# Kernel tuning notes

Measured on AMD Instinct MI355X. Metric: run time of the kernel, lower is better.

Reference implementation:

```python
import jax, jax.numpy as jnp
import numpy as np

B, C, H = 16, 512, 32
HID, NB, S, P, SR = 512, 36, 26, 7, 2
SCALE = 32.0
N_LOC, N_LOC_LAB = 12, 8
N_GRP, GRP_SZ, N_GRP_LAB = 4, 6, 16
IN_DIM = P * P * C


def roi_align(feat, coords, scale, pooled, sr):
    # feat: (B,C,H,W); coords: (B,NB,4) normalized xyxy. torchvision roi_align,
    # aligned=False, fixed sampling_ratio=sr (adaptive ratio is data-dependent).
    Bs, Cc, Hh, Ww = feat.shape
    x1 = coords[..., 0] * scale
    y1 = coords[..., 1] * scale
    x2 = coords[..., 2] * scale
    y2 = coords[..., 3] * scale
    rw = jnp.maximum(x2 - x1, 1.0)
    rh = jnp.maximum(y2 - y1, 1.0)
    bw = rw / pooled
    bh = rh / pooled
    # sample offsets within roi, in bin units: (pooled*sr,)
    off = (jnp.arange(pooled)[:, None] + (jnp.arange(sr) + 0.5) / sr).reshape(-1)
    ys = y1[..., None] + off * bh[..., None]  # (B,NB,pooled*sr)
    xs = x1[..., None] + off * bw[..., None]

    def prep(t, size):
        valid = (t > -1.0) & (t < size)
        tc = jnp.clip(t, 0.0, size - 1)
        lo = jnp.floor(tc).astype(jnp.int32)
        hi = jnp.minimum(lo + 1, size - 1)
        frac = tc - lo
        return lo, hi, frac, valid

    y_lo, y_hi, ly, vy = prep(ys, Hh)
    x_lo, x_hi, lx, vx = prep(xs, Ww)
    hy, hx = 1.0 - ly, 1.0 - lx

    featl = feat.transpose(0, 2, 3, 1)  # (B,H,W,C)
    b_idx = jnp.arange(Bs)[:, None, None, None]

    def gather(yi, xi):
        # -> (B,NB,Py,Px,C)
        return featl[b_idx, yi[:, :, :, None], xi[:, :, None, :]]

    def w(a, b):
        return (a[..., :, None] * b[..., None, :])[..., None]

    val = (gather(y_lo, x_lo) * w(hy, hx) + gather(y_lo, x_hi) * w(hy, lx)
           + gather(y_hi, x_lo) * w(ly, hx) + gather(y_hi, x_hi) * w(ly, lx))
    mask = (vy[:, :, :, None] & vx[:, :, None, :])[..., None]
    val = jnp.where(mask, val, 0.0)
    val = val.reshape(Bs, -1, pooled, sr, pooled, sr, Cc).mean(axis=(3, 5))
    return val.transpose(0, 1, 4, 2, 3)  # (B,NB,C,pooled,pooled)


def setup_inputs() -> dict:
    key = jax.random.key(0)
    ks = jax.random.split(key, 10)
    lf = jax.random.normal(ks[0], (B, C, H, H), dtype=jnp.float32)
    xs = jnp.sort(jax.random.uniform(ks[1], (B, S, 2)), axis=-1)
    ys = jnp.sort(jax.random.uniform(ks[2], (B, S, 2)), axis=-1)
    coords = jnp.stack([xs[..., 0], ys[..., 0], xs[..., 1], ys[..., 1]], axis=-1)
    sc = 0.02
    return {
        'local_features': lf,
        'pred_bbox_coords': coords,
        'roi_fc_W': jax.random.normal(ks[3], (HID, IN_DIM), dtype=jnp.float32) * sc,
        'roi_fc_b': jnp.zeros((HID,), jnp.float32),
        'coords_W': jax.random.normal(ks[4], (S, 4, HID), dtype=jnp.float32) * sc,
        'coords_b': jnp.zeros((S, 4), jnp.float32),
        'pres_W': jax.random.normal(ks[5], (S, HID), dtype=jnp.float32) * sc,
        'pres_b': jnp.zeros((S,), jnp.float32),
        'loc_W': jax.random.normal(ks[6], (N_LOC, N_LOC_LAB, HID), dtype=jnp.float32) * sc,
        'loc_b': jnp.zeros((N_LOC, N_LOC_LAB), jnp.float32),
        'grp_W': jax.random.normal(ks[7], (N_GRP, N_GRP_LAB, GRP_SZ * HID), dtype=jnp.float32) * sc,
        'grp_b': jnp.zeros((N_GRP, N_GRP_LAB), jnp.float32),
        'loc_idx': jnp.arange(N_LOC, dtype=jnp.int32),
        'grp_idx': jnp.arange(N_GRP * GRP_SZ, dtype=jnp.int32).reshape(N_GRP, GRP_SZ),
    }


def reference(local_features, pred_bbox_coords, roi_fc_W, roi_fc_b, coords_W,
              coords_b, pres_W, pres_b, loc_W, loc_b, grp_W, grp_b, loc_idx, grp_idx):
    Bs = local_features.shape[0]
    # boxes S..NB default to the full image (0,0,1,1)
    full = jnp.broadcast_to(jnp.array([0.0, 0.0, 1.0, 1.0], jnp.float32), (Bs, NB, 4))
    coords_all = full.at[:, :S].set(pred_bbox_coords)
    roi = roi_align(local_features, coords_all, SCALE, P, SR)  # (B,NB,C,P,P)
    flat = roi.reshape(Bs, NB, IN_DIM)
    feats = jax.nn.relu(jnp.einsum('bnf,hf->bnh', flat, roi_fc_W) + roi_fc_b)
    sup = feats[:, :S]  # (B,S,HID)
    # per-box coord refinement heads
    deltas = jnp.einsum('bsh,soh->bso', sup, coords_W) + coords_b  # (B,S,4)
    w = pred_bbox_coords[..., 2] - pred_bbox_coords[..., 0]
    h = pred_bbox_coords[..., 3] - pred_bbox_coords[..., 1]
    wh = jnp.stack([w, h, w, h], axis=-1)
    refined = pred_bbox_coords + deltas * wh
    presence = jnp.einsum('bsh,sh->bs', sup, pres_W) + pres_b  # (B,S)
    # per-box MLC heads
    loc = jnp.einsum('blh,loh->blo', feats[:, loc_idx], loc_W) + loc_b
    # per-group MLC heads (concat box feats within group along hidden)
    gf = feats[:, grp_idx].reshape(Bs, N_GRP, GRP_SZ * HID)
    grp = jnp.einsum('bgk,gok->bgo', gf, grp_W) + grp_b
    mlc = jnp.concatenate([loc.reshape(Bs, -1), grp.reshape(Bs, -1)], axis=1)
    return refined, presence, mlc
```

## Files before the change

kernel.cpp:

```cpp
#include <hip/hip_runtime.h>

typedef unsigned short u16;
typedef __attribute__((ext_vector_type(8))) short short8;
typedef __attribute__((ext_vector_type(8))) unsigned short ushort8_t;
typedef __attribute__((ext_vector_type(4))) float f32x4;
typedef __attribute__((ext_vector_type(2))) float v2f;

#define BATCH   16
#define CCH     512
#define NBOX    36
#define SS      26
#define INDIM   25088
#define HIDN    512
#define M_ROWS  416
#define KSPLIT  56
#define KITERS  7
#define NKB     392

__device__ __forceinline__ u16 f2bf(float f) {
  unsigned u = __float_as_uint(f);
  u += 0x7FFF + ((u >> 16) & 1);
  return (u16)(u >> 16);
}
__device__ __forceinline__ float bf2f(u16 h) {
  return __uint_as_float(((unsigned)h) << 16);
}
__device__ __forceinline__ v2f bf2x2(u16 a, u16 b) {
  v2f r;
  r.x = __uint_as_float(((unsigned)a) << 16);
  r.y = __uint_as_float(((unsigned)b) << 16);
  return r;
}

__global__ __launch_bounds__(256) void k_prep(const float* __restrict__ lf,
                                              const float* __restrict__ roiW,
                                              u16* __restrict__ lf_t,
                                              u16* __restrict__ Wb2) {
  __shared__ union {
    u16 tr[32][66];
    u16 cv[49 * 132];
  } sm;
  int j = blockIdx.x;
  int t = threadIdx.x;

  if (j < 4096) {
    int ct = j & 7, y = (j >> 3) & 31, b = j >> 8;
    int cl = t >> 2;
    int xq = (t & 3) * 8;
    const float* src = lf + ((size_t)(b * CCH + ct * 64 + cl) * 1024) + y * 32 + xq;
    float4 v0 = *(const float4*)src;
    float4 v1 = *(const float4*)(src + 4);
    sm.tr[xq + 0][cl] = f2bf(v0.x); sm.tr[xq + 1][cl] = f2bf(v0.y);
    sm.tr[xq + 2][cl] = f2bf(v0.z); sm.tr[xq + 3][cl] = f2bf(v0.w);
    sm.tr[xq + 4][cl] = f2bf(v1.x); sm.tr[xq + 5][cl] = f2bf(v1.y);
    sm.tr[xq + 6][cl] = f2bf(v1.z); sm.tr[xq + 7][cl] = f2bf(v1.w);
    __syncthreads();
    int xl = t >> 3;
    int cq = (t & 7) * 8;
    ushort8_t o;
#pragma unroll
    for (int i = 0; i < 8; ++i) o[i] = sm.tr[xl][cq + i];
    *(ushort8_t*)(lf_t + ((size_t)b * 1024 + y * 32 + xl) * CCH + ct * 64 + cq) = o;
  } else {
    int j2 = j - 4096;
    int h  = j2 >> 2;
    int c0 = (j2 & 3) * 128;
    const float4* s4 = (const float4*)(roiW + (size_t)h * INDIM + (size_t)c0 * 49);
    for (int i = t; i < 1568; i += 256) {
      float4 v = s4[i];
      int k = i * 4;
#pragma unroll
      for (int jj = 0; jj < 4; ++jj) {
        int kk = k + jj;
        int cc = kk / 49;
        int p  = kk - cc * 49;
        sm.cv[p * 132 + cc] = f2bf((&v.x)[jj]);
      }
    }
    __syncthreads();
    for (int q = t; q < 784; q += 256) {
      int p = q >> 4;
      int cc0 = (q & 15) * 8;
      const u16* sp = &sm.cv[p * 132 + cc0];
      ushort8_t o;
#pragma unroll
      for (int i = 0; i < 8; ++i) o[i] = sp[i];
      int c   = c0 + cc0;
      int kb  = p * 8 + (c >> 6);
      int col = c & 63;
      *(ushort8_t*)(Wb2 + ((size_t)kb * HIDN + h) * 64 + col) = o;
    }
  }
}

__global__ __launch_bounds__(512) void k_roi(const u16* __restrict__ lf_t,
                                             const float* __restrict__ pred,
                                             u16* __restrict__ flat2) {
  __shared__ int   s_ylo[14], s_yhi[14], s_xlo[14], s_xhi[14];
  __shared__ float s_wyl[14], s_wyh[14], s_wxl[14], s_wxh[14];

  int bid = blockIdx.x;
  int xcd = bid & 7;
  int s = bid >> 3;
  int b = xcd * 2 + (s >= 26 ? 1 : 0);
  int n = (s >= 26) ? s - 26 : s;
  int blk = b * 26 + n;
  int t = threadIdx.x;

  if (t < 28) {
    bool isY = t < 14;
    int j = isY ? t : t - 14;
    const float* p = pred + ((size_t)(b * SS + n)) * 4;
    float c0 = p[0], c1 = p[1], c2 = p[2], c3 = p[3];
    float lo1 = (isY ? c1 : c0) * 32.f;
    float hi1 = (isY ? c3 : c2) * 32.f;
    float sz = fmaxf(hi1 - lo1, 1.f);
    float bs = sz * (1.f / 7.f);
    float off = (float)(j >> 1) + 0.25f + 0.5f * (float)(j & 1);
    float pos = lo1 + off * bs;
    bool valid = (pos > -1.f) && (pos < 32.f);
    float tc = fminf(fmaxf(pos, 0.f), 31.f);
    int lo = (int)floorf(tc);
    int hi = min(lo + 1, 31);
    float fr = tc - (float)lo;
    float wl = valid ? (1.f - fr) : 0.f;
    float wh = valid ? fr : 0.f;
    if (isY) { s_ylo[j] = lo; s_yhi[j] = hi; s_wyl[j] = wl; s_wyh[j] = wh; }
    else     { s_xlo[j] = lo; s_xhi[j] = hi; s_wxl[j] = wl; s_wxh[j] = wh; }
  }
  __syncthreads();

  int cg = t & 63;
  int pg = t >> 6;
  const u16* base = lf_t + (size_t)b * 1024 * CCH + cg * 8;

  for (int p = pg; p < 49; p += 8) {
    int py = p / 7, px = p % 7;
    v2f a0 = {0.f, 0.f}, a1 = {0.f, 0.f}, a2 = {0.f, 0.f}, a3 = {0.f, 0.f};
#pragma unroll
    for (int sy = 0; sy < 2; ++sy) {
      int jy = 2 * py + sy;
      const u16* rlo = base + s_ylo[jy] * 32 * CCH;
      const u16* rhi = base + s_yhi[jy] * 32 * CCH;
      float wyl = s_wyl[jy], wyh = s_wyh[jy];
#pragma unroll
      for (int sx = 0; sx < 2; ++sx) {
        int jx = 2 * px + sx;
        int xl = s_xlo[jx] * CCH, xh = s_xhi[jx] * CCH;
        v2f wll = {wyl * s_wxl[jx], wyl * s_wxl[jx]};
        v2f wlh = {wyl * s_wxh[jx], wyl * s_wxh[jx]};
        v2f whl = {wyh * s_wxl[jx], wyh * s_wxl[jx]};
        v2f whh = {wyh * s_wxh[jx], wyh * s_wxh[jx]};
        ushort8_t vll = *(const ushort8_t*)(rlo + xl);
        ushort8_t vlh = *(const ushort8_t*)(rlo + xh);
        ushort8_t vhl = *(const ushort8_t*)(rhi + xl);
        ushort8_t vhh = *(const ushort8_t*)(rhi + xh);
        a0 += wll * bf2x2(vll[0], vll[1]) + wlh * bf2x2(vlh[0], vlh[1])
            + whl * bf2x2(vhl[0], vhl[1]) + whh * bf2x2(vhh[0], vhh[1]);
        a1 += wll * bf2x2(vll[2], vll[3]) + wlh * bf2x2(vlh[2], vlh[3])
            + whl * bf2x2(vhl[2], vhl[3]) + whh * bf2x2(vhh[2], vhh[3]);
        a2 += wll * bf2x2(vll[4], vll[5]) + wlh * bf2x2(vlh[4], vlh[5])
            + whl * bf2x2(vhl[4], vhl[5]) + whh * bf2x2(vhh[4], vhh[5]);
        a3 += wll * bf2x2(vll[6], vll[7]) + wlh * bf2x2(vlh[6], vlh[7])
            + whl * bf2x2(vhl[6], vhl[7]) + whh * bf2x2(vhh[6], vhh[7]);
      }
    }
    ushort8_t o;
    o[0] = f2bf(a0.x * 0.25f); o[1] = f2bf(a0.y * 0.25f);
    o[2] = f2bf(a1.x * 0.25f); o[3] = f2bf(a1.y * 0.25f);
    o[4] = f2bf(a2.x * 0.25f); o[5] = f2bf(a2.y * 0.25f);
    o[6] = f2bf(a3.x * 0.25f); o[7] = f2bf(a3.y * 0.25f);
    int kb = p * 8 + (cg >> 3);
    int col = (cg & 7) * 8;
    *(ushort8_t*)(flat2 + ((size_t)kb * M_ROWS + blk) * 64 + col) = o;
  }
}

__global__ __launch_bounds__(256) void k_gemm(const u16* __restrict__ flat2,
                                              const u16* __restrict__ Wb2,
                                              u16* __restrict__ partials) {
  __shared__ u16 As[128 * 64];
  __shared__ u16 Bs[128 * 64];

  int tid = threadIdx.x;
  int wave = tid >> 6, lane = tid & 63;
  int wm = wave >> 1, wn = wave & 1;
  int quad = lane >> 4, r = lane & 15;
  int xb = r & 7;

  int bid = blockIdx.x;
  int xcd = bid & 7;
  int slot = bid >> 3;
  int z = xcd * 7 + (slot >> 4);
  int xy = slot & 15;
  int tileN0 = (xy & 3) * 128;
  int tileM0 = (xy >> 2) * 128;
  int kb0 = z * KITERS;

  size_t aoff[4], boff[4];
  int    ldso[4];
#pragma unroll
  for (int t = 0; t < 4; ++t) {
    int chunk = (wave * 4 + t) * 64 + lane;
    int row = chunk >> 3;
    int lc = chunk & 7;
    ldso[t] = row * 64 + ((lc ^ (row & 7)) << 3);
    int grow = min(tileM0 + row, M_ROWS - 1);
    aoff[t] = ((size_t)kb0 * M_ROWS + grow) * 64 + lc * 8;
    boff[t] = ((size_t)kb0 * HIDN + tileN0 + row) * 64 + lc * 8;
  }

  f32x4 acc[4][4];
#pragma unroll
  for (int mi = 0; mi < 4; ++mi)
#pragma unroll
    for (int ni = 0; ni < 4; ++ni) acc[mi][ni] = (f32x4){0.f, 0.f, 0.f, 0.f};

  short8 ra[4], rb[4];
#pragma unroll
  for (int t = 0; t < 4; ++t) {
    ra[t] = *(const short8*)(flat2 + aoff[t]);
    rb[t] = *(const short8*)(Wb2 + boff[t]);
  }

  for (int kt = 0; kt < KITERS; ++kt) {
#pragma unroll
    for (int t = 0; t < 4; ++t) {
      *(short8*)&As[ldso[t]] = ra[t];
      *(short8*)&Bs[ldso[t]] = rb[t];
    }
    __syncthreads();

    if (kt + 1 < KITERS) {
      size_t ak = (size_t)(kt + 1) * (M_ROWS * 64);
      size_t bk = (size_t)(kt + 1) * (HIDN * 64);
#pragma unroll
      for (int t = 0; t < 4; ++t) {
        ra[t] = *(const short8*)(flat2 + aoff[t] + ak);
        rb[t] = *(const short8*)(Wb2 + boff[t] + bk);
      }
    }

#pragma unroll
    for (int kk = 0; kk < 64; kk += 32) {
      int k8 = kk >> 3;
      int pc = ((k8 + quad) ^ xb) << 3;
      short8 af[4], bfr[4];
#pragma unroll
      for (int mi = 0; mi < 4; ++mi)
        af[mi] = *(const short8*)&As[(wm * 64 + mi * 16 + r) * 64 + pc];
#pragma unroll
      for (int ni = 0; ni < 4; ++ni)
        bfr[ni] = *(const short8*)&Bs[(wn * 64 + ni * 16 + r) * 64 + pc];
#pragma unroll
      for (int mi = 0; mi < 4; ++mi)
#pragma unroll
        for (int ni = 0; ni < 4; ++ni)
          acc[mi][ni] = __builtin_amdgcn_mfma_f32_16x16x32_bf16(
              af[mi], bfr[ni], acc[mi][ni], 0, 0, 0);
    }
    __syncthreads();
  }

  u16* part = partials + (size_t)z * (M_ROWS * HIDN);
#pragma unroll
  for (int mi = 0; mi < 4; ++mi)
#pragma unroll
    for (int ni = 0; ni < 4; ++ni) {
      int row0 = tileM0 + wm * 64 + mi * 16 + quad * 4;
      int col = tileN0 + wn * 64 + ni * 16 + r;
#pragma unroll
      for (int reg = 0; reg < 4; ++reg) {
        int row = row0 + reg;
        if (row < M_ROWS) part[(size_t)row * HIDN + col] = f2bf(acc[mi][ni][reg]);
      }
    }
}

__global__ __launch_bounds__(256) void k_reduce(const u16* __restrict__ partials,
                                                const float* __restrict__ bias,
                                                float* __restrict__ feats) {
  int gid = blockIdx.x * 256 + threadIdx.x;
  int zh  = gid & 1;
  int idx = gid >> 1;
  int row = idx >> 6;
  int c0  = (idx & 63) * 8;
  float s[8] = {0.f, 0.f, 0.f, 0.f, 0.f, 0.f, 0.f, 0.f};
  const u16* p = partials + (size_t)row * HIDN + c0
               + (size_t)(zh * 28) * (M_ROWS * HIDN);
  for (int z = 0; z < 28; ++z) {
    ushort8_t v = *(const ushort8_t*)(p + (size_t)z * (M_ROWS * HIDN));
#pragma unroll
    for (int j = 0; j < 8; ++j) s[j] += bf2f(v[j]);
  }
#pragma unroll
  for (int j = 0; j < 8; ++j) s[j] += __shfl_xor(s[j], 1);
  if (zh == 0) {
    float4 o0, o1;
    const float* bi = bias + c0;
    o0.x = fmaxf(s[0] + bi[0], 0.f); o0.y = fmaxf(s[1] + bi[1], 0.f);
    o0.z = fmaxf(s[2] + bi[2], 0.f); o0.w = fmaxf(s[3] + bi[3], 0.f);
    o1.x = fmaxf(s[4] + bi[4], 0.f); o1.y = fmaxf(s[5] + bi[5], 0.f);
    o1.z = fmaxf(s[6] + bi[6], 0.f); o1.w = fmaxf(s[7] + bi[7], 0.f);
    float* dst = feats + (size_t)row * HIDN + c0;
    *(float4*)dst = o0;
    *(float4*)(dst + 4) = o1;
  }
}

__device__ __forceinline__ float wave_red(float s) {
#pragma unroll
  for (int off = 32; off > 0; off >>= 1) s += __shfl_down(s, off);
  return s;
}

__device__ __forceinline__ float dot512(const float* __restrict__ f,
                                        const float* __restrict__ w, int lane) {
  const float4* f4 = (const float4*)f;
  const float4* w4 = (const float4*)w;
  float4 x0 = f4[lane], y0 = w4[lane];
  float4 x1 = f4[lane + 64], y1 = w4[lane + 64];
  return x0.x * y0.x + x0.y * y0.y + x0.z * y0.z + x0.w * y0.w +
         x1.x * y1.x + x1.y * y1.y + x1.z * y1.z + x1.w * y1.w;
}

__global__ __launch_bounds__(256) void k_heads(const float* __restrict__ feats,
                                               const float* __restrict__ pred,
                                               const float* __restrict__ cW,
                                               const float* __restrict__ cb,
                                               const float* __restrict__ pW,
                                               const float* __restrict__ pb,
                                               const float* __restrict__ lW,
                                               const float* __restrict__ lb,
                                               const float* __restrict__ gW,
                                               const float* __restrict__ gb,
                                               const int* __restrict__ lidx,
                                               const int* __restrict__ gidx,
                                               float* __restrict__ out) {
  int wid = blockIdx.x * 4 + (threadIdx.x >> 6);
  int lane = threadIdx.x & 63;
  float sum = 0.f;

  if (wid < 1664) {
    int b = wid / 104, rr = wid % 104, s = rr >> 2, o = rr & 3;
    sum = dot512(feats + (size_t)(b * 26 + s) * HIDN,
                 cW + (size_t)(s * 4 + o) * HIDN, lane);
    sum = wave_red(sum);
    if (lane == 0) {
      const float* p = pred + (size_t)(b * SS + s) * 4;
      float wdt = p[2] - p[0], hgt = p[3] - p[1];
      float whv = (o & 1) ? hgt : wdt;
      out[wid] = p[o] + (sum + cb[s * 4 + o]) * whv;
    }
  } else if (wid < 2080) {
    int i = wid - 1664;
    int b = i / 26, s = i % 26;
    sum = dot512(feats + (size_t)(b * 26 + s) * HIDN,
                 pW + (size_t)s * HIDN, lane);
    sum = wave_red(sum);
    if (lane == 0) out[1664 + i] = sum + pb[s];
  } else if (wid < 3616) {
    int i = wid - 2080;
    int b = i / 96, rr = i % 96, l = rr >> 3, o = rr & 7;
    sum = dot512(feats + (size_t)(b * 26 + lidx[l]) * HIDN,
                 lW + (size_t)(l * 8 + o) * HIDN, lane);
    sum = wave_red(sum);
    if (lane == 0) out[2080 + b * 160 + rr] = sum + lb[l * 8 + o];
  } else {
    int i = wid - 3616;
    int b = i / 64, rr = i % 64, g = rr >> 4, o = rr & 15;
    const float* w = gW + (size_t)(g * 16 + o) * 3072;
#pragma unroll
    for (int jj = 0; jj < 6; ++jj) {
      sum += dot512(feats + (size_t)(b * 26 + gidx[g * 6 + jj]) * HIDN,
                    w + jj * 512, lane);
    }
    sum = wave_red(sum);
    if (lane == 0) out[2080 + b * 160 + 96 + rr] = sum + gb[g * 16 + o];
  }
}

extern "C" void kernel_launch(void* const* d_in, const int* in_sizes, int n_in,
                              void* d_out, int out_size, void* d_ws, size_t ws_size,
                              hipStream_t stream) {
  const float* lf      = (const float*)d_in[0];
  const float* pred    = (const float*)d_in[1];
  const float* roiW    = (const float*)d_in[2];
  const float* roiB    = (const float*)d_in[3];
  const float* cW      = (const float*)d_in[4];
  const float* cb      = (const float*)d_in[5];
  const float* pW      = (const float*)d_in[6];
  const float* pb      = (const float*)d_in[7];
  const float* lW      = (const float*)d_in[8];
  const float* lb      = (const float*)d_in[9];
  const float* gW      = (const float*)d_in[10];
  const float* gb      = (const float*)d_in[11];
  const int*   lidx    = (const int*)d_in[12];
  const int*   gidx    = (const int*)d_in[13];
  float* out = (float*)d_out;

  char* ws = (char*)d_ws;
  u16*   lf_t     = (u16*)ws;
  u16*   partials = (u16*)ws;
  u16*   Wb2   = (u16*)(ws + 33030144);
  u16*   flat2 = (u16*)(ws + 33030144 + 25690112);
  float* feats = (float*)(ws + 33030144 + 25690112 + 28901376);

  k_prep<<<6144, 256, 0, stream>>>(lf, roiW, lf_t, Wb2);
  k_roi<<<M_ROWS, 512, 0, stream>>>(lf_t, pred, flat2);
  k_gemm<<<896, 256, 0, stream>>>(flat2, Wb2, partials);
  k_reduce<<<208, 256, 0, stream>>>(partials, roiB, feats);
  k_heads<<<1160, 256, 0, stream>>>(feats, pred, cW, cb, pW, pb, lW, lb, gW, gb,
                                    lidx, gidx, out);
}
```

Baseline: 192.4 us.

## Fuse ROI-align into prep kernel with per-batch semaphores for overlap

Merges the ROI-align kernel into the transpose/convert prep kernel. ROI blocks spin on a per-batch atomic counter until all 256 transpose blocks for that batch have finished, and each box is split into two half-blocks. The W conversion blocks are placed after the ROI blocks so they can overlap the wait. This removes a kernel launch boundary and lets ROI work start per batch, at the cost of a memset launch and spin-wait blocks that depend on the scheduler dispatching blocks in order.

```diff
diff --git a/kernel.cpp b/kernel.cpp
--- a/kernel.cpp
+++ b/kernel.cpp
@@ -32,13 +32,20 @@
   return r;
 }
 
-__global__ __launch_bounds__(256) void k_prep(const float* __restrict__ lf,
-                                              const float* __restrict__ roiW,
-                                              u16* __restrict__ lf_t,
-                                              u16* __restrict__ Wb2) {
+__global__ __launch_bounds__(256) void k_prep_roi(const float* __restrict__ lf,
+                                                  const float* __restrict__ roiW,
+                                                  const float* __restrict__ pred,
+                                                  u16* __restrict__ lf_t,
+                                                  u16* __restrict__ Wb2,
+                                                  u16* __restrict__ flat2,
+                                                  unsigned* __restrict__ sem) {
   __shared__ union {
     u16 tr[32][66];
     u16 cv[49 * 132];
+    struct {
+      int   ylo[14], yhi[14], xlo[14], xhi[14];
+      float wyl[14], wyh[14], wxl[14], wxh[14];
+    } roi;
   } sm;
   int j = blockIdx.x;
   int t = threadIdx.x;
@@ -61,8 +68,102 @@
 #pragma unroll
     for (int i = 0; i < 8; ++i) o[i] = sm.tr[xl][cq + i];
     *(ushort8_t*)(lf_t + ((size_t)b * 1024 + y * 32 + xl) * CCH + ct * 64 + cq) = o;
+    __syncthreads();
+    if (t == 0) {
+      __threadfence();
+      __hip_atomic_fetch_add(sem + b * 32, 1u,
+                             __ATOMIC_RELAXED, __HIP_MEMORY_SCOPE_AGENT);
+    }
+  } else if (j < 4928) {
+    int jj = j - 4096;
+    int half = (jj >= 416) ? 1 : 0;
+    int bj   = half ? jj - 416 : jj;
+    int xcd  = bj & 7;
+    int s    = bj >> 3;
+    int b    = xcd * 2 + (s >= 26 ? 1 : 0);
+    int n    = (s >= 26) ? s - 26 : s;
+    int blk  = b * 26 + n;
+
+    if (t == 0) {
+      while (__hip_atomic_load(sem + b * 32, __ATOMIC_RELAXED,
+                               __HIP_MEMORY_SCOPE_AGENT) < 256u)
+        __builtin_amdgcn_s_sleep(16);
+      __threadfence();
+    }
+    __syncthreads();
+
+    if (t < 28) {
+      bool isY = t < 14;
+      int jt = isY ? t : t - 14;
+      const float* pp = pred + ((size_t)(b * SS + n)) * 4;
+      float c0 = pp[0], c1 = pp[1], c2 = pp[2], c3 = pp[3];
+      float lo1 = (isY ? c1 : c0) * 32.f;
+      float hi1 = (isY ? c3 : c2) * 32.f;
+      float sz = fmaxf(hi1 - lo1, 1.f);
+      float bs = sz * (1.f / 7.f);
+      float off = (float)(jt >> 1) + 0.25f + 0.5f * (float)(jt & 1);
+      float pos = lo1 + off * bs;
+      bool valid = (pos > -1.f) && (pos < 32.f);
+      float tc = fminf(fmaxf(pos, 0.f), 31.f);
+      int lo = (int)floorf(tc);
+      int hi = min(lo + 1, 31);
+      float fr = tc - (float)lo;
+      float wl = valid ? (1.f - fr) : 0.f;
+      float wh = valid ? fr : 0.f;
+      if (isY) { sm.roi.ylo[jt] = lo; sm.roi.yhi[jt] = hi;
+                 sm.roi.wyl[jt] = wl; sm.roi.wyh[jt] = wh; }
+      else     { sm.roi.xlo[jt] = lo; sm.roi.xhi[jt] = hi;
+                 sm.roi.wxl[jt] = wl; sm.roi.wxh[jt] = wh; }
+    }
+    __syncthreads();
+
+    int cgi = t & 63;
+    int pg  = t >> 6;
+    const u16* base = lf_t + (size_t)b * 1024 * CCH + cgi * 8;
+    int pend = half ? 49 : 24;
+
+    for (int p = (half ? 24 : 0) + pg; p < pend; p += 4) {
+      int py = p / 7, px = p % 7;
+      v2f a0 = {0.f, 0.f}, a1 = {0.f, 0.f}, a2 = {0.f, 0.f}, a3 = {0.f, 0.f};
+#pragma unroll
+      for (int sy = 0; sy < 2; ++sy) {
+        int jy = 2 * py + sy;
+        const u16* rlo = base + sm.roi.ylo[jy] * 32 * CCH;
+        const u16* rhi = base + sm.roi.yhi[jy] * 32 * CCH;
+        float wyl = sm.roi.wyl[jy], wyh = sm.roi.wyh[jy];
+#pragma unroll
+        for (int sx = 0; sx < 2; ++sx) {
+          int jx = 2 * px + sx;
+          int xl = sm.roi.xlo[jx] * CCH, xh = sm.roi.xhi[jx] * CCH;
+          v2f wll = {wyl * sm.roi.wxl[jx], wyl * sm.roi.wxl[jx]};
+          v2f wlh = {wyl * sm.roi.wxh[jx], wyl * sm.roi.wxh[jx]};
+          v2f whl = {wyh * sm.roi.wxl[jx], wyh * sm.roi.wxl[jx]};
+          v2f whh = {wyh * sm.roi.wxh[jx], wyh * sm.roi.wxh[jx]};
+          ushort8_t vll = *(const ushort8_t*)(rlo + xl);
+          ushort8_t vlh = *(const ushort8_t*)(rlo + xh);
+          ushort8_t vhl = *(const ushort8_t*)(rhi + xl);
+          ushort8_t vhh = *(const ushort8_t*)(rhi + xh);
+          a0 += wll * bf2x2(vll[0], vll[1]) + wlh * bf2x2(vlh[0], vlh[1])
+              + whl * bf2x2(vhl[0], vhl[1]) + whh * bf2x2(vhh[0], vhh[1]);
+          a1 += wll * bf2x2(vll[2], vll[3]) + wlh * bf2x2(vlh[2], vlh[3])
+              + whl * bf2x2(vhl[2], vhl[3]) + whh * bf2x2(vhh[2], vhh[3]);
+          a2 += wll * bf2x2(vll[4], vll[5]) + wlh * bf2x2(vlh[4], vlh[5])
+              + whl * bf2x2(vhl[4], vhl[5]) + whh * bf2x2(vhh[4], vhh[5]);
+          a3 += wll * bf2x2(vll[6], vll[7]) + wlh * bf2x2(vlh[6], vlh[7])
+              + whl * bf2x2(vhl[6], vhl[7]) + whh * bf2x2(vhh[6], vhh[7]);
+        }
+      }
+      ushort8_t o;
+      o[0] = f2bf(a0.x * 0.25f); o[1] = f2bf(a0.y * 0.25f);
+      o[2] = f2bf(a1.x * 0.25f); o[3] = f2bf(a1.y * 0.25f);
+      o[4] = f2bf(a2.x * 0.25f); o[5] = f2bf(a2.y * 0.25f);
+      o[6] = f2bf(a3.x * 0.25f); o[7] = f2bf(a3.y * 0.25f);
+      int kb  = p * 8 + (cgi >> 3);
+      int col = (cgi & 7) * 8;
+      *(ushort8_t*)(flat2 + ((size_t)kb * M_ROWS + blk) * 64 + col) = o;
+    }
   } else {
-    int j2 = j - 4096;
+    int j2 = j - 4928;
     int h  = j2 >> 2;
     int c0 = (j2 & 3) * 128;
     const float4* s4 = (const float4*)(roiW + (size_t)h * INDIM + (size_t)c0 * 49);
@@ -90,89 +191,6 @@
       int col = c & 63;
       *(ushort8_t*)(Wb2 + ((size_t)kb * HIDN + h) * 64 + col) = o;
     }
-  }
-}
-
-__global__ __launch_bounds__(512) void k_roi(const u16* __restrict__ lf_t,
-                                             const float* __restrict__ pred,
-                                             u16* __restrict__ flat2) {
-  __shared__ int   s_ylo[14], s_yhi[14], s_xlo[14], s_xhi[14];
-  __shared__ float s_wyl[14], s_wyh[14], s_wxl[14], s_wxh[14];
-
-  int bid = blockIdx.x;
-  int xcd = bid & 7;
-  int s = bid >> 3;
-  int b = xcd * 2 + (s >= 26 ? 1 : 0);
-  int n = (s >= 26) ? s - 26 : s;
-  int blk = b * 26 + n;
-  int t = threadIdx.x;
-
-  if (t < 28) {
-    bool isY = t < 14;
-    int j = isY ? t : t - 14;
-    const float* p = pred + ((size_t)(b * SS + n)) * 4;
-    float c0 = p[0], c1 = p[1], c2 = p[2], c3 = p[3];
-    float lo1 = (isY ? c1 : c0) * 32.f;
-    float hi1 = (isY ? c3 : c2) * 32.f;
-    float sz = fmaxf(hi1 - lo1, 1.f);
-    float bs = sz * (1.f / 7.f);
-    float off = (float)(j >> 1) + 0.25f + 0.5f * (float)(j & 1);
-    float pos = lo1 + off * bs;
-    bool valid = (pos > -1.f) && (pos < 32.f);
-    float tc = fminf(fmaxf(pos, 0.f), 31.f);
-    int lo = (int)floorf(tc);
-    int hi = min(lo + 1, 31);
-    float fr = tc - (float)lo;
-    float wl = valid ? (1.f - fr) : 0.f;
-    float wh = valid ? fr : 0.f;
-    if (isY) { s_ylo[j] = lo; s_yhi[j] = hi; s_wyl[j] = wl; s_wyh[j] = wh; }
-    else     { s_xlo[j] = lo; s_xhi[j] = hi; s_wxl[j] = wl; s_wxh[j] = wh; }
-  }
-  __syncthreads();
-
-  int cg = t & 63;
-  int pg = t >> 6;
-  const u16* base = lf_t + (size_t)b * 1024 * CCH + cg * 8;
-
-  for (int p = pg; p < 49; p += 8) {
-    int py = p / 7, px = p % 7;
-    v2f a0 = {0.f, 0.f}, a1 = {0.f, 0.f}, a2 = {0.f, 0.f}, a3 = {0.f, 0.f};
-#pragma unroll
-    for (int sy = 0; sy < 2; ++sy) {
-      int jy = 2 * py + sy;
-      const u16* rlo = base + s_ylo[jy] * 32 * CCH;
-      const u16* rhi = base + s_yhi[jy] * 32 * CCH;
-      float wyl = s_wyl[jy], wyh = s_wyh[jy];
-#pragma unroll
-      for (int sx = 0; sx < 2; ++sx) {
-        int jx = 2 * px + sx;
-        int xl = s_xlo[jx] * CCH, xh = s_xhi[jx] * CCH;
-        v2f wll = {wyl * s_wxl[jx], wyl * s_wxl[jx]};
-        v2f wlh = {wyl * s_wxh[jx], wyl * s_wxh[jx]};
-        v2f whl = {wyh * s_wxl[jx], wyh * s_wxl[jx]};
-        v2f whh = {wyh * s_wxh[jx], wyh * s_wxh[jx]};
-        ushort8_t vll = *(const ushort8_t*)(rlo + xl);
-        ushort8_t vlh = *(const ushort8_t*)(rlo + xh);
-        ushort8_t vhl = *(const ushort8_t*)(rhi + xl);
-        ushort8_t vhh = *(const ushort8_t*)(rhi + xh);
-        a0 += wll * bf2x2(vll[0], vll[1]) + wlh * bf2x2(vlh[0], vlh[1])
-            + whl * bf2x2(vhl[0], vhl[1]) + whh * bf2x2(vhh[0], vhh[1]);
-        a1 += wll * bf2x2(vll[2], vll[3]) + wlh * bf2x2(vlh[2], vlh[3])
-            + whl * bf2x2(vhl[2], vhl[3]) + whh * bf2x2(vhh[2], vhh[3]);
-        a2 += wll * bf2x2(vll[4], vll[5]) + wlh * bf2x2(vlh[4], vlh[5])
-            + whl * bf2x2(vhl[4], vhl[5]) + whh * bf2x2(vhh[4], vhh[5]);
-        a3 += wll * bf2x2(vll[6], vll[7]) + wlh * bf2x2(vlh[6], vlh[7])
-            + whl * bf2x2(vhl[6], vhl[7]) + whh * bf2x2(vhh[6], vhh[7]);
-      }
-    }
-    ushort8_t o;
-    o[0] = f2bf(a0.x * 0.25f); o[1] = f2bf(a0.y * 0.25f);
-    o[2] = f2bf(a1.x * 0.25f); o[3] = f2bf(a1.y * 0.25f);
-    o[4] = f2bf(a2.x * 0.25f); o[5] = f2bf(a2.y * 0.25f);
-    o[6] = f2bf(a3.x * 0.25f); o[7] = f2bf(a3.y * 0.25f);
-    int kb = p * 8 + (cg >> 3);
-    int col = (cg & 7) * 8;
-    *(ushort8_t*)(flat2 + ((size_t)kb * M_ROWS + blk) * 64 + col) = o;
   }
 }
 
@@ -404,10 +422,11 @@
   u16*   partials = (u16*)ws;
   u16*   Wb2   = (u16*)(ws + 33030144);
   u16*   flat2 = (u16*)(ws + 33030144 + 25690112);
+  unsigned* sem = (unsigned*)(ws + 33030144 + 25690112 + 20873216);
   float* feats = (float*)(ws + 33030144 + 25690112 + 28901376);
 
-  k_prep<<<6144, 256, 0, stream>>>(lf, roiW, lf_t, Wb2);
-  k_roi<<<M_ROWS, 512, 0, stream>>>(lf_t, pred, flat2);
+  hipMemsetAsync((void*)sem, 0, 2048, stream);
+  k_prep_roi<<<6976, 256, 0, stream>>>(lf, roiW, pred, lf_t, Wb2, flat2, sem);
   k_gemm<<<896, 256, 0, stream>>>(flat2, Wb2, partials);
   k_reduce<<<208, 256, 0, stream>>>(partials, roiB, feats);
   k_heads<<<1160, 256, 0, stream>>>(feats, pred, cW, cb, pW, pb, lW, lb, gW, gb,
```

Measured after the change: 377.7 us. +96.3%, slower.
